# Performance work log

Hardware: AMD Instinct MI355X
Metric: run time of the kernel (lower is better)

Reference implementation:

```python
import jax, jax.numpy as jnp
import numpy as np

N = 100000      # nodes
E = 1600000     # edges
DIM = 64        # feat_channel
H = 4           # heads
C = DIM // H    # per-head channels
L = 3           # layer_num
G = 16          # graphs in batch
NCLS = 2
NEG_SLOPE_ATT = 0.2   # GATConv leaky relu
NEG_SLOPE_ACT = 0.01  # 'Leaky' activation
EPS = 1e-5


def setup_inputs() -> dict:
    key = jax.random.key(0)
    ks = jax.random.split(key, 8)
    x = jax.random.normal(ks[0], (N, DIM), dtype=jnp.float32)
    edge_index = jax.random.randint(ks[1], (2, E), 0, N, dtype=jnp.int32)
    batch = jnp.sort(jax.random.randint(ks[2], (N,), 0, G, dtype=jnp.int32))
    W = jax.random.normal(ks[3], (L, DIM, DIM), dtype=jnp.float32) / np.sqrt(DIM)
    att_src = jax.random.normal(ks[4], (L, H, C), dtype=jnp.float32) * 0.1
    att_dst = jax.random.normal(ks[5], (L, H, C), dtype=jnp.float32) * 0.1
    bias = jnp.zeros((L, DIM), dtype=jnp.float32)
    gamma = jnp.ones((L, DIM), dtype=jnp.float32)
    beta = jnp.zeros((L, DIM), dtype=jnp.float32)
    Wr = jax.random.normal(ks[6], ((L + 1) * DIM, NCLS), dtype=jnp.float32) / np.sqrt((L + 1) * DIM)
    br = jnp.zeros((NCLS,), dtype=jnp.float32)
    return {"x": x, "edge_index": edge_index, "batch": batch, "n_graphs": G,
            "W": W, "att_src": att_src, "att_dst": att_dst, "bias": bias,
            "gamma": gamma, "beta": beta, "Wr": Wr, "br": br}


def _gat_conv(x, src, dst, W_l, a_src, a_dst, b_l):
    # x: [N, DIM] -> h: [N, H, C]
    h = (x @ W_l).reshape(-1, H, C)
    # per-node attention logits [N, H]
    e_src = jnp.einsum('nhc,hc->nh', h, a_src)
    e_dst = jnp.einsum('nhc,hc->nh', h, a_dst)
    alpha = jax.nn.leaky_relu(e_src[src] + e_dst[dst], NEG_SLOPE_ATT)  # [E, H]
    # segment softmax over incoming edges of each destination node
    amax = jax.ops.segment_max(alpha, dst, num_segments=N)
    ex = jnp.exp(alpha - amax[dst])
    den = jax.ops.segment_sum(ex, dst, num_segments=N)
    att = ex / (den[dst] + 1e-16)                                      # [E, H]
    # weighted scatter aggregation
    msg = h[src] * att[:, :, None]                                     # [E, H, C]
    out = jax.ops.segment_sum(msg, dst, num_segments=N)
    return out.reshape(-1, H * C) + b_l, att


def _batch_norm(x, g, b):
    mu = jnp.mean(x, axis=0)
    var = jnp.var(x, axis=0)
    return (x - mu) * jax.lax.rsqrt(var + EPS) * g + b


def _mean_pool(x, batch, n_graphs, cnt):
    return jax.ops.segment_sum(x, batch, num_segments=n_graphs) / cnt[:, None]


def reference(x, edge_index, batch, n_graphs, W, att_src, att_dst, bias, gamma, beta, Wr, br):
    src, dst = edge_index[0], edge_index[1]
    cnt = jax.ops.segment_sum(jnp.ones((x.shape[0],), x.dtype), batch,
                              num_segments=n_graphs)                   # nodes per graph
    inv_sqrt_n = jax.lax.rsqrt(cnt)[batch][:, None]                    # GraphSizeNorm factor

    x_out = x
    pools = [_mean_pool(x, batch, n_graphs, cnt)]                      # x0_glob
    for l in range(L):
        h, _att = _gat_conv(x_out, src, dst, W[l], att_src[l], att_dst[l], bias[l])
        h = _batch_norm(h, gamma[l], beta[l]) * inv_sqrt_n             # BatchNorm + GraphSizeNorm
        h = jax.nn.leaky_relu(h, NEG_SLOPE_ACT)
        pools.append(_mean_pool(h, batch, n_graphs, cnt))
        x_out = h + x_out                                              # residual 'Y'

    x_concat = jnp.concatenate(pools, axis=1)                          # [G, (L+1)*DIM]
    risk = x_concat @ Wr + br                                          # [G, NCLS]
    Y_prob = jax.nn.softmax(risk, axis=1)
    Y_hat = jnp.argmax(risk, axis=1)
    return risk, Y_prob, Y_hat
```

## Files before the change

kernel.cpp:

```cpp
#include <hip/hip_runtime.h>

constexpr int NN   = 100000;
constexpr int EE   = 1600000;
constexpr int DIM  = 64;
constexpr int HH   = 4;
constexpr int CC   = 16;
constexpr int LL   = 3;
constexpr int GG   = 16;
constexpr int NCLS = 2;
constexpr float SLOPE_ATT = 0.2f;
constexpr float SLOPE_ACT = 0.01f;
constexpr float EPS = 1e-5f;

constexpr int SCAN_CHUNK = 1024;
constexpr int NSCAN = (NN + SCAN_CHUNK - 1) / SCAN_CHUNK;
constexpr int NREP = 64;

typedef int vint4 __attribute__((ext_vector_type(4)));

__device__ __forceinline__ float lrelu_att(float v) { return v > 0.f ? v : SLOPE_ATT * v; }
__device__ __forceinline__ float lrelu_act(float v) { return v > 0.f ? v : SLOPE_ACT * v; }

__device__ __forceinline__ unsigned short f2bf(float f) {
    unsigned u = __float_as_uint(f);
    unsigned r = u + 0x7FFFu + ((u >> 16) & 1u);
    return (unsigned short)(r >> 16);
}
__device__ __forceinline__ float bflo(unsigned u) { return __uint_as_float(u << 16); }
__device__ __forceinline__ float bfhi(unsigned u) { return __uint_as_float(u & 0xFFFF0000u); }

__global__ __launch_bounds__(256) void k_hist(const int* __restrict__ ei,
                                              int* __restrict__ deg) {
    int i = blockIdx.x * 256 + threadIdx.x;
    if (i < EE / 4) {
        vint4 d = __builtin_nontemporal_load(&((const vint4*)(ei + EE))[i]);
        atomicAdd(&deg[d.x], 1);
        atomicAdd(&deg[d.y], 1);
        atomicAdd(&deg[d.z], 1);
        atomicAdd(&deg[d.w], 1);
    }
}

__global__ __launch_bounds__(256) void k_scan1(const int* __restrict__ deg,
                                               int* __restrict__ excl,
                                               int* __restrict__ bsum) {
    __shared__ int sh[256];
    const int b = blockIdx.x, t = threadIdx.x;
    const int i0 = b * SCAN_CHUNK + t * 4;
    int v[4];
#pragma unroll
    for (int i = 0; i < 4; ++i) v[i] = (i0 + i < NN) ? deg[i0 + i] : 0;
    int tsum = v[0] + v[1] + v[2] + v[3];
    sh[t] = tsum;
    __syncthreads();
    for (int o = 1; o < 256; o <<= 1) {
        int x = (t >= o) ? sh[t - o] : 0;
        __syncthreads();
        sh[t] += x;
        __syncthreads();
    }
    if (t == 255) bsum[b] = sh[255];
    int run = sh[t] - tsum;
#pragma unroll
    for (int i = 0; i < 4; ++i) {
        if (i0 + i < NN) excl[i0 + i] = run;
        run += v[i];
    }
}

__global__ void k_scan2(const int* __restrict__ bsum, int* __restrict__ bsum_sc) {
    __shared__ int sh[128];
    const int t = threadIdx.x;
    const int own = (t < NSCAN) ? bsum[t] : 0;
    sh[t] = own;
    __syncthreads();
    for (int o = 1; o < 128; o <<= 1) {
        int x = (t >= o) ? sh[t - o] : 0;
        __syncthreads();
        sh[t] += x;
        __syncthreads();
    }
    if (t < NSCAN) bsum_sc[t] = sh[t] - own;
}

__global__ __launch_bounds__(256) void k_scan3(int* __restrict__ row_start,
                                               const int* __restrict__ bsum_sc,
                                               int* __restrict__ cursor) {
    int i = blockIdx.x * 256 + threadIdx.x;
    if (i < NN) {
        int v = row_start[i] + bsum_sc[i / SCAN_CHUNK];
        row_start[i] = v;
        cursor[i] = v;
    }
    if (i == 0) row_start[NN] = EE;
}

constexpr int FILL_NBLK = 256;
constexpr int DRANGE = (NN + 7) / 8;
__global__ __launch_bounds__(256) void k_fill(const int* __restrict__ ei,
                                              int* __restrict__ cursor,
                                              int* __restrict__ ssrc) {
    const int g = blockIdx.x & 7;
    const int blk = blockIdx.x >> 3;
    const int dlo = g * DRANGE, dhi = min(dlo + DRANGE, NN);
    const int stride = FILL_NBLK * 256;
    for (int e = blk * 256 + threadIdx.x; e < EE; e += stride) {
        int d = __builtin_nontemporal_load(&ei[EE + e]);
        if (d >= dlo && d < dhi) {
            int s = __builtin_nontemporal_load(&ei[e]);
            int pos = atomicAdd(&cursor[d], 1);
            ssrc[pos] = s;
        }
    }
}

template<int MODE>
__global__ __launch_bounds__(256) void k_gemm_t(const float* __restrict__ xbase,
                                                const float* __restrict__ aggin,
                                                const float* __restrict__ scshf,
                                                const int* __restrict__ batch,
                                                const float* __restrict__ cntin,
                                                const float* __restrict__ Wl,
                                                const float* __restrict__ asrc,
                                                const float* __restrict__ adst,
                                                float* __restrict__ xcur_out,
                                                unsigned short* __restrict__ h,
                                                float* __restrict__ es,
                                                float* __restrict__ ed,
                                                double* __restrict__ bnrep,
                                                float* __restrict__ poolout,
                                                float* __restrict__ cntout) {
    if (blockIdx.x < NREP && threadIdx.x < 128)
        bnrep[(size_t)blockIdx.x * 128 + threadIdx.x] = 0.0;
    __shared__ float Ws[DIM][DIM];
    __shared__ float xsT[DIM][DIM];
    __shared__ float sp[GG * 64];
    __shared__ float scnt[GG];
    const int tid = threadIdx.x;
    const int row0 = blockIdx.x * 64;

    for (int i = tid; i < GG * 64; i += 256) sp[i] = 0.f;
    if (MODE == 0 && tid < GG) scnt[tid] = 0.f;
    __syncthreads();

    const float4* W4 = (const float4*)Wl;
#pragma unroll
    for (int i = 0; i < 4; ++i) ((float4*)Ws)[tid + 256 * i] = W4[tid + 256 * i];

    const int c4_ = tid & 15;
    float4 scv, shfv;
    if (MODE == 1) {
        scv  = ((const float4*)scshf)[c4_];
        shfv = ((const float4*)scshf)[16 + c4_];
    }

#pragma unroll
    for (int i = 0; i < 4; ++i) {
        int idx4 = tid + 256 * i;
        int r = idx4 >> 4, c4 = idx4 & 15;
        int grow = row0 + r;
        float4 v4 = make_float4(0.f, 0.f, 0.f, 0.f);
        if (grow < NN) {
            if (MODE == 0) {
                v4 = ((const float4*)xbase)[grow * 16 + c4];
                int g = batch[grow];
                atomicAdd(&sp[g * 64 + c4 * 4 + 0], v4.x);
                atomicAdd(&sp[g * 64 + c4 * 4 + 1], v4.y);
                atomicAdd(&sp[g * 64 + c4 * 4 + 2], v4.z);
                atomicAdd(&sp[g * 64 + c4 * 4 + 3], v4.w);
                if (c4 == 0) atomicAdd(&scnt[g], 1.f);
            } else {
                float4 a4 = ((const float4*)aggin)[grow * 16 + c4];
                float4 xb = ((const float4*)xbase)[grow * 16 + c4];
                int g = batch[grow];
                float rinv = rsqrtf(cntin[g]);
                float vx = lrelu_act((a4.x * scv.x + shfv.x) * rinv);
                float vy = lrelu_act((a4.y * scv.y + shfv.y) * rinv);
                float vz = lrelu_act((a4.z * scv.z + shfv.z) * rinv);
                float vw = lrelu_act((a4.w * scv.w + shfv.w) * rinv);
                atomicAdd(&sp[g * 64 + c4 * 4 + 0], vx);
                atomicAdd(&sp[g * 64 + c4 * 4 + 1], vy);
                atomicAdd(&sp[g * 64 + c4 * 4 + 2], vz);
                atomicAdd(&sp[g * 64 + c4 * 4 + 3], vw);
                v4 = make_float4(xb.x + vx, xb.y + vy, xb.z + vz, xb.w + vw);
                ((float4*)xcur_out)[grow * 16 + c4] = v4;
            }
        }
        int col = (((r >> 2) ^ c4) << 2) | (r & 3);
        xsT[c4 * 4 + 0][col] = v4.x;
        xsT[c4 * 4 + 1][col] = v4.y;
        xsT[c4 * 4 + 2][col] = v4.z;
        xsT[c4 * 4 + 3][col] = v4.w;
    }
    __syncthreads();

    const int tc = tid & 15, tr = tid >> 4;
    float acc[4][4] = {};
#pragma unroll 8
    for (int k = 0; k < DIM; ++k) {
        int kc = (k >> 2) & 15;
        float4 wv = *(const float4*)(&Ws[k][tc * 4]);
        float4 xv = *(const float4*)(&xsT[k][(tr ^ kc) * 4]);
        acc[0][0] = fmaf(xv.x, wv.x, acc[0][0]);
        acc[0][1] = fmaf(xv.x, wv.y, acc[0][1]);
        acc[0][2] = fmaf(xv.x, wv.z, acc[0][2]);
        acc[0][3] = fmaf(xv.x, wv.w, acc[0][3]);
        acc[1][0] = fmaf(xv.y, wv.x, acc[1][0]);
        acc[1][1] = fmaf(xv.y, wv.y, acc[1][1]);
        acc[1][2] = fmaf(xv.y, wv.z, acc[1][2]);
        acc[1][3] = fmaf(xv.y, wv.w, acc[1][3]);
        acc[2][0] = fmaf(xv.z, wv.x, acc[2][0]);
        acc[2][1] = fmaf(xv.z, wv.y, acc[2][1]);
        acc[2][2] = fmaf(xv.z, wv.z, acc[2][2]);
        acc[2][3] = fmaf(xv.z, wv.w, acc[2][3]);
        acc[3][0] = fmaf(xv.w, wv.x, acc[3][0]);
        acc[3][1] = fmaf(xv.w, wv.y, acc[3][1]);
        acc[3][2] = fmaf(xv.w, wv.z, acc[3][2]);
        acc[3][3] = fmaf(xv.w, wv.w, acc[3][3]);
    }

    float a_s[4], a_d[4];
#pragma unroll
    for (int c = 0; c < 4; ++c) { a_s[c] = asrc[4 * tc + c]; a_d[c] = adst[4 * tc + c]; }

#pragma unroll
    for (int r = 0; r < 4; ++r) {
        int n = row0 + 4 * tr + r;
        if (n < NN) {
            ushort4 hb;
            hb.x = f2bf(acc[r][0]); hb.y = f2bf(acc[r][1]);
            hb.z = f2bf(acc[r][2]); hb.w = f2bf(acc[r][3]);
            *(ushort4*)(h + n * 64 + 4 * tc) = hb;
            float ps = acc[r][0] * a_s[0] + acc[r][1] * a_s[1] +
                       acc[r][2] * a_s[2] + acc[r][3] * a_s[3];
            float pd = acc[r][0] * a_d[0] + acc[r][1] * a_d[1] +
                       acc[r][2] * a_d[2] + acc[r][3] * a_d[3];
            ps += __shfl_xor(ps, 1); ps += __shfl_xor(ps, 2);
            pd += __shfl_xor(pd, 1); pd += __shfl_xor(pd, 2);
            if ((tc & 3) == 0) {
                es[n * 4 + (tc >> 2)] = ps;
                ed[n * 4 + (tc >> 2)] = pd;
            }
        }
    }

    for (int i = tid; i < GG * 64; i += 256)
        if (sp[i] != 0.f) atomicAdd(&poolout[i], sp[i]);
    if (MODE == 0 && tid < GG && scnt[tid] != 0.f) atomicAdd(&cntout[tid], scnt[tid]);
}

__global__ __launch_bounds__(256) void k_gat_agg(const int* __restrict__ row_start,
                                                 const int* __restrict__ ssrc,
                                                 const float* __restrict__ es,
                                                 const float* __restrict__ ed,
                                                 const unsigned short* __restrict__ h,
                                                 float* __restrict__ agg,
                                                 double* __restrict__ bnrep) {
    __shared__ int   sbuf[16][34];
    __shared__ float exbuf[16][34][4];
    __shared__ float stS[4][64];
    __shared__ float stQ[4][64];

    const int lane16 = threadIdx.x & 15;
    const int grp    = threadIdx.x >> 4;
    const int wid    = threadIdx.x >> 6;
    const int sub    = lane16 >> 3;
    const int l8     = lane16 & 7;
    const int hq8    = l8 >> 1;
    const int n = blockIdx.x * 16 + grp;
    const int base = row_start[n];
    const int deg  = row_start[n + 1] - base;
    const float4 edv = *(const float4*)(ed + n * 4);
    const uint4* h16 = (const uint4*)h;

    float acc8[8] = {};
    float4 denp = make_float4(0.f, 0.f, 0.f, 0.f);

    if (deg <= 32) {
        int s0 = 0, s1 = 0;
        float4 al0 = make_float4(-INFINITY, -INFINITY, -INFINITY, -INFINITY);
        float4 al1 = al0;
        if (lane16 < deg) {
            s0 = ssrc[base + lane16];
            float4 ev = *(const float4*)(es + s0 * 4);
            al0.x = lrelu_att(ev.x + edv.x); al0.y = lrelu_att(ev.y + edv.y);
            al0.z = lrelu_att(ev.z + edv.z); al0.w = lrelu_att(ev.w + edv.w);
        }
        if (lane16 + 16 < deg) {
            s1 = ssrc[base + 16 + lane16];
            float4 ev = *(const float4*)(es + s1 * 4);
            al1.x = lrelu_att(ev.x + edv.x); al1.y = lrelu_att(ev.y + edv.y);
            al1.z = lrelu_att(ev.z + edv.z); al1.w = lrelu_att(ev.w + edv.w);
        }
        float4 mx = make_float4(fmaxf(al0.x, al1.x), fmaxf(al0.y, al1.y),
                                fmaxf(al0.z, al1.z), fmaxf(al0.w, al1.w));
#pragma unroll
        for (int o = 1; o < 16; o <<= 1) {
            mx.x = fmaxf(mx.x, __shfl_xor(mx.x, o));
            mx.y = fmaxf(mx.y, __shfl_xor(mx.y, o));
            mx.z = fmaxf(mx.z, __shfl_xor(mx.z, o));
            mx.w = fmaxf(mx.w, __shfl_xor(mx.w, o));
        }
        float4 ex0 = make_float4(0.f, 0.f, 0.f, 0.f), ex1 = ex0;
        if (lane16 < deg) {
            ex0.x = __expf(al0.x - mx.x); ex0.y = __expf(al0.y - mx.y);
            ex0.z = __expf(al0.z - mx.z); ex0.w = __expf(al0.w - mx.w);
        }
        if (lane16 + 16 < deg) {
            ex1.x = __expf(al1.x - mx.x); ex1.y = __expf(al1.y - mx.y);
            ex1.z = __expf(al1.z - mx.z); ex1.w = __expf(al1.w - mx.w);
        }
        denp.x = ex0.x + ex1.x; denp.y = ex0.y + ex1.y;
        denp.z = ex0.z + ex1.z; denp.w = ex0.w + ex1.w;
        sbuf[grp][lane16] = s0;
        sbuf[grp][lane16 + 16] = s1;
        *(float4*)&exbuf[grp][lane16][0] = ex0;
        *(float4*)&exbuf[grp][lane16 + 16][0] = ex1;
        const int dceil = (deg + 1) & ~1;
#pragma unroll 4
        for (int i = 0; i < dceil; i += 2) {
            int si = sbuf[grp][i + sub];
            float e = exbuf[grp][i + sub][hq8];
            uint4 hv = h16[si * 8 + l8];
            acc8[0] = fmaf(e, bflo(hv.x), acc8[0]);
            acc8[1] = fmaf(e, bfhi(hv.x), acc8[1]);
            acc8[2] = fmaf(e, bflo(hv.y), acc8[2]);
            acc8[3] = fmaf(e, bfhi(hv.y), acc8[3]);
            acc8[4] = fmaf(e, bflo(hv.z), acc8[4]);
            acc8[5] = fmaf(e, bfhi(hv.z), acc8[5]);
            acc8[6] = fmaf(e, bflo(hv.w), acc8[6]);
            acc8[7] = fmaf(e, bfhi(hv.w), acc8[7]);
        }
    } else {
        float4 mx = make_float4(-INFINITY, -INFINITY, -INFINITY, -INFINITY);
        for (int c0 = 0; c0 < deg; c0 += 16) {
            if (c0 + lane16 < deg) {
                int s = ssrc[base + c0 + lane16];
                float4 ev = *(const float4*)(es + s * 4);
                mx.x = fmaxf(mx.x, lrelu_att(ev.x + edv.x));
                mx.y = fmaxf(mx.y, lrelu_att(ev.y + edv.y));
                mx.z = fmaxf(mx.z, lrelu_att(ev.z + edv.z));
                mx.w = fmaxf(mx.w, lrelu_att(ev.w + edv.w));
            }
        }
#pragma unroll
        for (int o = 1; o < 16; o <<= 1) {
            mx.x = fmaxf(mx.x, __shfl_xor(mx.x, o));
            mx.y = fmaxf(mx.y, __shfl_xor(mx.y, o));
            mx.z = fmaxf(mx.z, __shfl_xor(mx.z, o));
            mx.w = fmaxf(mx.w, __shfl_xor(mx.w, o));
        }
        for (int c0 = 0; c0 < deg; c0 += 16) {
            int cn = min(16, deg - c0);
            float4 ex = make_float4(0.f, 0.f, 0.f, 0.f);
            int s = 0;
            if (lane16 < cn) {
                s = ssrc[base + c0 + lane16];
                float4 ev = *(const float4*)(es + s * 4);
                ex.x = __expf(lrelu_att(ev.x + edv.x) - mx.x);
                ex.y = __expf(lrelu_att(ev.y + edv.y) - mx.y);
                ex.z = __expf(lrelu_att(ev.z + edv.z) - mx.z);
                ex.w = __expf(lrelu_att(ev.w + edv.w) - mx.w);
            }
            denp.x += ex.x; denp.y += ex.y; denp.z += ex.z; denp.w += ex.w;
            sbuf[grp][lane16] = s;
            *(float4*)&exbuf[grp][lane16][0] = ex;
            const int pc = (cn + 1) & ~1;
            for (int i = 0; i < pc; i += 2) {
                int si = sbuf[grp][i + sub];
                float e = exbuf[grp][i + sub][hq8];
                uint4 hv = h16[si * 8 + l8];
                acc8[0] = fmaf(e, bflo(hv.x), acc8[0]);
                acc8[1] = fmaf(e, bfhi(hv.x), acc8[1]);
                acc8[2] = fmaf(e, bflo(hv.y), acc8[2]);
                acc8[3] = fmaf(e, bfhi(hv.y), acc8[3]);
                acc8[4] = fmaf(e, bflo(hv.z), acc8[4]);
                acc8[5] = fmaf(e, bfhi(hv.z), acc8[5]);
                acc8[6] = fmaf(e, bflo(hv.w), acc8[6]);
                acc8[7] = fmaf(e, bfhi(hv.w), acc8[7]);
            }
        }
    }

#pragma unroll
    for (int q = 0; q < 8; ++q) acc8[q] += __shfl_xor(acc8[q], 8);
#pragma unroll
    for (int o = 1; o < 16; o <<= 1) {
        denp.x += __shfl_xor(denp.x, o);
        denp.y += __shfl_xor(denp.y, o);
        denp.z += __shfl_xor(denp.z, o);
        denp.w += __shfl_xor(denp.w, o);
    }
    float dh = hq8 == 0 ? denp.x : hq8 == 1 ? denp.y : hq8 == 2 ? denp.z : denp.w;
    float inv = 1.f / (dh + 1e-16f);
    float o8[8];
#pragma unroll
    for (int q = 0; q < 8; ++q) o8[q] = acc8[q] * inv;

    if (sub == 0) {
        *(float4*)(agg + n * 64 + l8 * 8)     = make_float4(o8[0], o8[1], o8[2], o8[3]);
        *(float4*)(agg + n * 64 + l8 * 8 + 4) = make_float4(o8[4], o8[5], o8[6], o8[7]);
    }

    float sv[8], qv[8];
#pragma unroll
    for (int q = 0; q < 8; ++q) {
        float v = (sub == 0) ? o8[q] : 0.f;
        sv[q] = v; qv[q] = v * v;
    }
#pragma unroll
    for (int q = 0; q < 8; ++q) {
        sv[q] += __shfl_xor(sv[q], 16); sv[q] += __shfl_xor(sv[q], 32);
        qv[q] += __shfl_xor(qv[q], 16); qv[q] += __shfl_xor(qv[q], 32);
    }
    if ((threadIdx.x & 63) < 8) {
        *(float4*)&stS[wid][l8 * 8]     = make_float4(sv[0], sv[1], sv[2], sv[3]);
        *(float4*)&stS[wid][l8 * 8 + 4] = make_float4(sv[4], sv[5], sv[6], sv[7]);
        *(float4*)&stQ[wid][l8 * 8]     = make_float4(qv[0], qv[1], qv[2], qv[3]);
        *(float4*)&stQ[wid][l8 * 8 + 4] = make_float4(qv[4], qv[5], qv[6], qv[7]);
    }
    __syncthreads();
    if (threadIdx.x < 64) {
        int j = threadIdx.x;
        float ssum = stS[0][j] + stS[1][j] + stS[2][j] + stS[3][j];
        float qsum = stQ[0][j] + stQ[1][j] + stQ[2][j] + stQ[3][j];
        double* rep = bnrep + (size_t)(blockIdx.x & (NREP - 1)) * 128;
        atomicAdd(&rep[j], (double)ssum);
        atomicAdd(&rep[64 + j], (double)qsum);
    }
}

__global__ void k_bn_final(const double* __restrict__ bnrep,
                           const float* __restrict__ gamma,
                           const float* __restrict__ beta,
                           float* __restrict__ scshf) {
    int j = threadIdx.x;
    if (j < 64) {
        double s1 = 0.0, s2 = 0.0;
        for (int rp = 0; rp < NREP; ++rp) {
            s1 += bnrep[(size_t)rp * 128 + j];
            s2 += bnrep[(size_t)rp * 128 + 64 + j];
        }
        double mean = s1 / (double)NN;
        double var = s2 / (double)NN - mean * mean;
        float sc = (float)(1.0 / sqrt(var + (double)EPS)) * gamma[j];
        scshf[j] = sc;
        scshf[64 + j] = beta[j] - (float)mean * sc;
    }
}

constexpr int NA_BLOCKS = 512;
constexpr int NA_NODES = (NN + NA_BLOCKS - 1) / NA_BLOCKS;
__global__ __launch_bounds__(256) void k_pool_final(const float* __restrict__ agg,
                                                    const float* __restrict__ scshf,
                                                    const int* __restrict__ batch,
                                                    const float* __restrict__ cnt,
                                                    float* __restrict__ pool) {
    __shared__ float sp[GG * 64];
    for (int i = threadIdx.x; i < GG * 64; i += 256) sp[i] = 0.f;
    __syncthreads();
    const int j = threadIdx.x & 63, r = threadIdx.x >> 6;
    const float sc = scshf[j], shf = scshf[64 + j];
    const int n0 = blockIdx.x * NA_NODES;
    const int n1 = min(n0 + NA_NODES, NN);
    float racc = 0.f;
    int curg = -1;
    float rinv = 0.f;
    for (int n = n0 + r; n < n1; n += 4) {
        int g = batch[n];
        if (g != curg) {
            if (curg >= 0) atomicAdd(&sp[curg * 64 + j], racc);
            curg = g; racc = 0.f;
            rinv = rsqrtf(cnt[g]);
        }
        float v = (agg[n * 64 + j] * sc + shf) * rinv;
        racc += lrelu_act(v);
    }
    if (curg >= 0) atomicAdd(&sp[curg * 64 + j], racc);
    __syncthreads();
    for (int i = threadIdx.x; i < GG * 64; i += 256)
        if (sp[i] != 0.f) atomicAdd(&pool[i], sp[i]);
}

__global__ void k_head(const float* __restrict__ pools,
                       const float* __restrict__ cnt,
                       const float* __restrict__ Wr,
                       const float* __restrict__ br,
                       float* __restrict__ out) {
    __shared__ float risk[GG * NCLS];
    int t = threadIdx.x;
    if (t < GG * NCLS) {
        int g = t / NCLS, c = t % NCLS;
        float acc = br[c];
        float icnt = 1.f / cnt[g];
        for (int k = 0; k < (LL + 1) * DIM; ++k) {
            int l = k >> 6, j = k & 63;
            float xc = pools[(l * GG + g) * 64 + j] * icnt;
            acc += xc * Wr[k * NCLS + c];
        }
        risk[t] = acc;
        out[t] = acc;
    }
    __syncthreads();
    if (t < GG) {
        float r0 = risk[t * 2], r1 = risk[t * 2 + 1];
        float m = fmaxf(r0, r1);
        float e0 = expf(r0 - m), e1 = expf(r1 - m);
        float s = e0 + e1;
        out[GG * NCLS + t * 2] = e0 / s;
        out[GG * NCLS + t * 2 + 1] = e1 / s;
        out[2 * GG * NCLS + t] = (r1 > r0) ? 1.f : 0.f;
    }
}

extern "C" void kernel_launch(void* const* d_in, const int* in_sizes, int n_in,
                              void* d_out, int out_size, void* d_ws, size_t ws_size,
                              hipStream_t stream) {
    const float* x     = (const float*)d_in[0];
    const int*   ei    = (const int*)d_in[1];
    const int*   batch = (const int*)d_in[2];
    const float* W     = (const float*)d_in[4];
    const float* asrc  = (const float*)d_in[5];
    const float* adst  = (const float*)d_in[6];
    const float* gamma = (const float*)d_in[8];
    const float* beta  = (const float*)d_in[9];
    const float* Wr    = (const float*)d_in[10];
    const float* br    = (const float*)d_in[11];
    float* out = (float*)d_out;

    char* ws = (char*)d_ws;
    size_t off = 0;
    auto alloc = [&](size_t bytes) {
        void* p = ws + off;
        off += (bytes + 255) & ~(size_t)255;
        return p;
    };
    float*          xcur      = (float*)alloc((size_t)NN * 64 * 4);
    unsigned short* h         = (unsigned short*)alloc((size_t)NN * 64 * 2);
    float*          agg       = (float*)alloc((size_t)NN * 64 * 4);
    float*          es        = (float*)alloc((size_t)NN * 4 * 4);
    float*          ed        = (float*)alloc((size_t)NN * 4 * 4);
    int*            row_start = (int*)alloc((size_t)(NN + 1) * 4);
    int*            ssrc      = (int*)alloc((size_t)EE * 4);
    double*         bnrep     = (double*)alloc((size_t)NREP * 128 * 8);
    float*          scshf     = (float*)alloc(128 * 4);
    float*          pools     = (float*)alloc((size_t)(LL + 1) * GG * 64 * 4);
    float*          cnt       = (float*)alloc((size_t)GG * 4);
    (void)ws_size; (void)in_sizes; (void)n_in; (void)out_size;

    int* deg     = (int*)agg;
    int* cursor  = (int*)agg + NN;
    int* bsum    = (int*)agg + 2 * NN;
    int* bsum_sc = (int*)agg + 2 * NN + 256;

    hipMemsetAsync(pools, 0, (size_t)(LL + 1) * GG * 64 * 4, stream);
    hipMemsetAsync(cnt, 0, (size_t)GG * 4, stream);
    hipMemsetAsync(deg, 0, (size_t)NN * 4, stream);

    k_hist<<<(EE / 4 + 255) / 256, 256, 0, stream>>>(ei, deg);
    k_scan1<<<NSCAN, 256, 0, stream>>>(deg, row_start, bsum);
    k_scan2<<<1, 128, 0, stream>>>(bsum, bsum_sc);
    k_scan3<<<(NN + 255) / 256, 256, 0, stream>>>(row_start, bsum_sc, cursor);
    k_fill<<<8 * FILL_NBLK, 256, 0, stream>>>(ei, cursor, ssrc);

    const int GEMM_GRID = (NN + 63) / 64;

    k_gemm_t<0><<<GEMM_GRID, 256, 0, stream>>>(x, nullptr, nullptr, batch, nullptr,
                                               W, asrc, adst, nullptr,
                                               h, es, ed, bnrep, pools, cnt);
    k_gat_agg<<<NN / 16, 256, 0, stream>>>(row_start, ssrc, es, ed, h, agg, bnrep);
    k_bn_final<<<1, 64, 0, stream>>>(bnrep, gamma, beta, scshf);

    k_gemm_t<1><<<GEMM_GRID, 256, 0, stream>>>(x, agg, scshf, batch, cnt,
                                               W + DIM * DIM, asrc + HH * CC, adst + HH * CC,
                                               xcur, h, es, ed, bnrep,
                                               pools + GG * 64, nullptr);
    k_gat_agg<<<NN / 16, 256, 0, stream>>>(row_start, ssrc, es, ed, h, agg, bnrep);
    k_bn_final<<<1, 64, 0, stream>>>(bnrep, gamma + DIM, beta + DIM, scshf);

    k_gemm_t<1><<<GEMM_GRID, 256, 0, stream>>>(xcur, agg, scshf, batch, cnt,
                                               W + 2 * DIM * DIM, asrc + 2 * HH * CC,
                                               adst + 2 * HH * CC,
                                               xcur, h, es, ed, bnrep,
                                               pools + 2 * GG * 64, nullptr);
    k_gat_agg<<<NN / 16, 256, 0, stream>>>(row_start, ssrc, es, ed, h, agg, bnrep);
    k_bn_final<<<1, 64, 0, stream>>>(bnrep, gamma + 2 * DIM, beta + 2 * DIM, scshf);

    k_pool_final<<<NA_BLOCKS, 256, 0, stream>>>(agg, scshf, batch, cnt,
                                                pools + 3 * GG * 64);

    k_head<<<1, 64, 0, stream>>>(pools, cnt, Wr, br, out);
}
```

Baseline: 595.4 us.

## Store node features as FP8 for gather, merge scan kernels, widen fill grid

Node features h are now packed to FP8 with hardware pack instructions instead of BF16, halving the bytes gathered per edge in the aggregation kernel. The aggregation is remapped so each 16-lane group processes four edges per step with 16 accumulators per lane, followed by an extra shuffle reduction. The two small scan kernels are merged into one that has thread 0 serially sum the block prefix, the two memsets are combined, and the fill grid is doubled. FP8 lowers feature precision substantially, which risks accuracy tolerance failures.

```diff
diff --git a/kernel.cpp b/kernel.cpp
--- a/kernel.cpp
+++ b/kernel.cpp
@@ -17,17 +17,10 @@
 constexpr int NREP = 64;
 
 typedef int vint4 __attribute__((ext_vector_type(4)));
+typedef float f32x2 __attribute__((ext_vector_type(2)));
 
 __device__ __forceinline__ float lrelu_att(float v) { return v > 0.f ? v : SLOPE_ATT * v; }
 __device__ __forceinline__ float lrelu_act(float v) { return v > 0.f ? v : SLOPE_ACT * v; }
-
-__device__ __forceinline__ unsigned short f2bf(float f) {
-    unsigned u = __float_as_uint(f);
-    unsigned r = u + 0x7FFFu + ((u >> 16) & 1u);
-    return (unsigned short)(r >> 16);
-}
-__device__ __forceinline__ float bflo(unsigned u) { return __uint_as_float(u << 16); }
-__device__ __forceinline__ float bfhi(unsigned u) { return __uint_as_float(u & 0xFFFF0000u); }
 
 __global__ __launch_bounds__(256) void k_hist(const int* __restrict__ ei,
                                               int* __restrict__ deg) {
@@ -68,34 +61,31 @@
     }
 }
 
-__global__ void k_scan2(const int* __restrict__ bsum, int* __restrict__ bsum_sc) {
+__global__ __launch_bounds__(256) void k_scan23(int* __restrict__ row_start,
+                                                const int* __restrict__ bsum,
+                                                int* __restrict__ cursor) {
     __shared__ int sh[128];
+    __shared__ int prefix;
     const int t = threadIdx.x;
-    const int own = (t < NSCAN) ? bsum[t] : 0;
-    sh[t] = own;
-    __syncthreads();
-    for (int o = 1; o < 128; o <<= 1) {
-        int x = (t >= o) ? sh[t - o] : 0;
-        __syncthreads();
-        sh[t] += x;
-        __syncthreads();
-    }
-    if (t < NSCAN) bsum_sc[t] = sh[t] - own;
-}
-
-__global__ __launch_bounds__(256) void k_scan3(int* __restrict__ row_start,
-                                               const int* __restrict__ bsum_sc,
-                                               int* __restrict__ cursor) {
-    int i = blockIdx.x * 256 + threadIdx.x;
+    if (t < NSCAN) sh[t] = bsum[t];
+    __syncthreads();
+    if (t == 0) {
+        int ci = blockIdx.x >> 2;
+        int p = 0;
+        for (int k = 0; k < ci; ++k) p += sh[k];
+        prefix = p;
+    }
+    __syncthreads();
+    int i = blockIdx.x * 256 + t;
     if (i < NN) {
-        int v = row_start[i] + bsum_sc[i / SCAN_CHUNK];
+        int v = row_start[i] + prefix;
         row_start[i] = v;
         cursor[i] = v;
     }
     if (i == 0) row_start[NN] = EE;
 }
 
-constexpr int FILL_NBLK = 256;
+constexpr int FILL_NBLK = 512;
 constexpr int DRANGE = (NN + 7) / 8;
 __global__ __launch_bounds__(256) void k_fill(const int* __restrict__ ei,
                                               int* __restrict__ cursor,
@@ -124,7 +114,7 @@
                                                 const float* __restrict__ asrc,
                                                 const float* __restrict__ adst,
                                                 float* __restrict__ xcur_out,
-                                                unsigned short* __restrict__ h,
+                                                unsigned* __restrict__ h32,
                                                 float* __restrict__ es,
                                                 float* __restrict__ ed,
                                                 double* __restrict__ bnrep,
@@ -227,10 +217,10 @@
     for (int r = 0; r < 4; ++r) {
         int n = row0 + 4 * tr + r;
         if (n < NN) {
-            ushort4 hb;
-            hb.x = f2bf(acc[r][0]); hb.y = f2bf(acc[r][1]);
-            hb.z = f2bf(acc[r][2]); hb.w = f2bf(acc[r][3]);
-            *(ushort4*)(h + n * 64 + 4 * tc) = hb;
+            int p = 0;
+            p = __builtin_amdgcn_cvt_pk_fp8_f32(acc[r][0], acc[r][1], p, false);
+            p = __builtin_amdgcn_cvt_pk_fp8_f32(acc[r][2], acc[r][3], p, true);
+            h32[n * 16 + tc] = (unsigned)p;
             float ps = acc[r][0] * a_s[0] + acc[r][1] * a_s[1] +
                        acc[r][2] * a_s[2] + acc[r][3] * a_s[3];
             float pd = acc[r][0] * a_d[0] + acc[r][1] * a_d[1] +
@@ -249,11 +239,31 @@
     if (MODE == 0 && tid < GG && scnt[tid] != 0.f) atomicAdd(&cntout[tid], scnt[tid]);
 }
 
+__device__ __forceinline__ void acc_fp8(float acc16[16], float e, uint4 hv) {
+    f32x2 p;
+    p = __builtin_amdgcn_cvt_pk_f32_fp8((int)hv.x, false);
+    acc16[0] = fmaf(e, p.x, acc16[0]);  acc16[1] = fmaf(e, p.y, acc16[1]);
+    p = __builtin_amdgcn_cvt_pk_f32_fp8((int)hv.x, true);
+    acc16[2] = fmaf(e, p.x, acc16[2]);  acc16[3] = fmaf(e, p.y, acc16[3]);
+    p = __builtin_amdgcn_cvt_pk_f32_fp8((int)hv.y, false);
+    acc16[4] = fmaf(e, p.x, acc16[4]);  acc16[5] = fmaf(e, p.y, acc16[5]);
+    p = __builtin_amdgcn_cvt_pk_f32_fp8((int)hv.y, true);
+    acc16[6] = fmaf(e, p.x, acc16[6]);  acc16[7] = fmaf(e, p.y, acc16[7]);
+    p = __builtin_amdgcn_cvt_pk_f32_fp8((int)hv.z, false);
+    acc16[8] = fmaf(e, p.x, acc16[8]);  acc16[9] = fmaf(e, p.y, acc16[9]);
+    p = __builtin_amdgcn_cvt_pk_f32_fp8((int)hv.z, true);
+    acc16[10] = fmaf(e, p.x, acc16[10]); acc16[11] = fmaf(e, p.y, acc16[11]);
+    p = __builtin_amdgcn_cvt_pk_f32_fp8((int)hv.w, false);
+    acc16[12] = fmaf(e, p.x, acc16[12]); acc16[13] = fmaf(e, p.y, acc16[13]);
+    p = __builtin_amdgcn_cvt_pk_f32_fp8((int)hv.w, true);
+    acc16[14] = fmaf(e, p.x, acc16[14]); acc16[15] = fmaf(e, p.y, acc16[15]);
+}
+
 __global__ __launch_bounds__(256) void k_gat_agg(const int* __restrict__ row_start,
                                                  const int* __restrict__ ssrc,
                                                  const float* __restrict__ es,
                                                  const float* __restrict__ ed,
-                                                 const unsigned short* __restrict__ h,
+                                                 const unsigned* __restrict__ h32,
                                                  float* __restrict__ agg,
                                                  double* __restrict__ bnrep) {
     __shared__ int   sbuf[16][34];
@@ -264,16 +274,15 @@
     const int lane16 = threadIdx.x & 15;
     const int grp    = threadIdx.x >> 4;
     const int wid    = threadIdx.x >> 6;
-    const int sub    = lane16 >> 3;
-    const int l8     = lane16 & 7;
-    const int hq8    = l8 >> 1;
+    const int sub    = lane16 >> 2;
+    const int l4     = lane16 & 3;
     const int n = blockIdx.x * 16 + grp;
     const int base = row_start[n];
     const int deg  = row_start[n + 1] - base;
     const float4 edv = *(const float4*)(ed + n * 4);
-    const uint4* h16 = (const uint4*)h;
-
-    float acc8[8] = {};
+    const uint4* h128 = (const uint4*)h32;
+
+    float acc16[16] = {};
     float4 denp = make_float4(0.f, 0.f, 0.f, 0.f);
 
     if (deg <= 32) {
@@ -316,20 +325,13 @@
         sbuf[grp][lane16 + 16] = s1;
         *(float4*)&exbuf[grp][lane16][0] = ex0;
         *(float4*)&exbuf[grp][lane16 + 16][0] = ex1;
-        const int dceil = (deg + 1) & ~1;
+        const int dceil = (deg + 3) & ~3;
 #pragma unroll 4
-        for (int i = 0; i < dceil; i += 2) {
+        for (int i = 0; i < dceil; i += 4) {
             int si = sbuf[grp][i + sub];
-            float e = exbuf[grp][i + sub][hq8];
-            uint4 hv = h16[si * 8 + l8];
-            acc8[0] = fmaf(e, bflo(hv.x), acc8[0]);
-            acc8[1] = fmaf(e, bfhi(hv.x), acc8[1]);
-            acc8[2] = fmaf(e, bflo(hv.y), acc8[2]);
-            acc8[3] = fmaf(e, bfhi(hv.y), acc8[3]);
-            acc8[4] = fmaf(e, bflo(hv.z), acc8[4]);
-            acc8[5] = fmaf(e, bfhi(hv.z), acc8[5]);
-            acc8[6] = fmaf(e, bflo(hv.w), acc8[6]);
-            acc8[7] = fmaf(e, bfhi(hv.w), acc8[7]);
+            float e = exbuf[grp][i + sub][l4];
+            uint4 hv = h128[si * 4 + l4];
+            acc_fp8(acc16, e, hv);
         }
     } else {
         float4 mx = make_float4(-INFINITY, -INFINITY, -INFINITY, -INFINITY);
@@ -365,25 +367,21 @@
             denp.x += ex.x; denp.y += ex.y; denp.z += ex.z; denp.w += ex.w;
             sbuf[grp][lane16] = s;
             *(float4*)&exbuf[grp][lane16][0] = ex;
-            const int pc = (cn + 1) & ~1;
-            for (int i = 0; i < pc; i += 2) {
+            const int pc = (cn + 3) & ~3;
+            for (int i = 0; i < pc; i += 4) {
                 int si = sbuf[grp][i + sub];
-                float e = exbuf[grp][i + sub][hq8];
-                uint4 hv = h16[si * 8 + l8];
-                acc8[0] = fmaf(e, bflo(hv.x), acc8[0]);
-                acc8[1] = fmaf(e, bfhi(hv.x), acc8[1]);
-                acc8[2] = fmaf(e, bflo(hv.y), acc8[2]);
-                acc8[3] = fmaf(e, bfhi(hv.y), acc8[3]);
-                acc8[4] = fmaf(e, bflo(hv.z), acc8[4]);
-                acc8[5] = fmaf(e, bfhi(hv.z), acc8[5]);
-                acc8[6] = fmaf(e, bflo(hv.w), acc8[6]);
-                acc8[7] = fmaf(e, bfhi(hv.w), acc8[7]);
+                float e = exbuf[grp][i + sub][l4];
+                uint4 hv = h128[si * 4 + l4];
+                acc_fp8(acc16, e, hv);
             }
         }
     }
 
 #pragma unroll
-    for (int q = 0; q < 8; ++q) acc8[q] += __shfl_xor(acc8[q], 8);
+    for (int q = 0; q < 16; ++q) {
+        acc16[q] += __shfl_xor(acc16[q], 4);
+        acc16[q] += __shfl_xor(acc16[q], 8);
+    }
 #pragma unroll
     for (int o = 1; o < 16; o <<= 1) {
         denp.x += __shfl_xor(denp.x, o);
@@ -391,33 +389,38 @@
         denp.z += __shfl_xor(denp.z, o);
         denp.w += __shfl_xor(denp.w, o);
     }
-    float dh = hq8 == 0 ? denp.x : hq8 == 1 ? denp.y : hq8 == 2 ? denp.z : denp.w;
+    float dh = l4 == 0 ? denp.x : l4 == 1 ? denp.y : l4 == 2 ? denp.z : denp.w;
     float inv = 1.f / (dh + 1e-16f);
-    float o8[8];
-#pragma unroll
-    for (int q = 0; q < 8; ++q) o8[q] = acc8[q] * inv;
-
-    if (sub == 0) {
-        *(float4*)(agg + n * 64 + l8 * 8)     = make_float4(o8[0], o8[1], o8[2], o8[3]);
-        *(float4*)(agg + n * 64 + l8 * 8 + 4) = make_float4(o8[4], o8[5], o8[6], o8[7]);
-    }
-
-    float sv[8], qv[8];
-#pragma unroll
-    for (int q = 0; q < 8; ++q) {
-        float v = (sub == 0) ? o8[q] : 0.f;
+    float o16[16];
+#pragma unroll
+    for (int q = 0; q < 16; ++q) o16[q] = acc16[q] * inv;
+
+    if (lane16 < 4) {
+#pragma unroll
+        for (int q4 = 0; q4 < 4; ++q4)
+            *(float4*)(agg + n * 64 + lane16 * 16 + q4 * 4) =
+                make_float4(o16[q4 * 4], o16[q4 * 4 + 1], o16[q4 * 4 + 2], o16[q4 * 4 + 3]);
+    }
+
+    float sv[16], qv[16];
+#pragma unroll
+    for (int q = 0; q < 16; ++q) {
+        float v = (lane16 < 4) ? o16[q] : 0.f;
         sv[q] = v; qv[q] = v * v;
     }
 #pragma unroll
-    for (int q = 0; q < 8; ++q) {
+    for (int q = 0; q < 16; ++q) {
         sv[q] += __shfl_xor(sv[q], 16); sv[q] += __shfl_xor(sv[q], 32);
         qv[q] += __shfl_xor(qv[q], 16); qv[q] += __shfl_xor(qv[q], 32);
     }
-    if ((threadIdx.x & 63) < 8) {
-        *(float4*)&stS[wid][l8 * 8]     = make_float4(sv[0], sv[1], sv[2], sv[3]);
-        *(float4*)&stS[wid][l8 * 8 + 4] = make_float4(sv[4], sv[5], sv[6], sv[7]);
-        *(float4*)&stQ[wid][l8 * 8]     = make_float4(qv[0], qv[1], qv[2], qv[3]);
-        *(float4*)&stQ[wid][l8 * 8 + 4] = make_float4(qv[4], qv[5], qv[6], qv[7]);
+    if ((threadIdx.x & 63) < 4) {
+#pragma unroll
+        for (int q4 = 0; q4 < 4; ++q4) {
+            *(float4*)&stS[wid][l4 * 16 + q4 * 4] =
+                make_float4(sv[q4 * 4], sv[q4 * 4 + 1], sv[q4 * 4 + 2], sv[q4 * 4 + 3]);
+            *(float4*)&stQ[wid][l4 * 16 + q4 * 4] =
+                make_float4(qv[q4 * 4], qv[q4 * 4 + 1], qv[q4 * 4 + 2], qv[q4 * 4 + 3]);
+        }
     }
     __syncthreads();
     if (threadIdx.x < 64) {
@@ -535,55 +538,52 @@
         off += (bytes + 255) & ~(size_t)255;
         return p;
     };
-    float*          xcur      = (float*)alloc((size_t)NN * 64 * 4);
-    unsigned short* h         = (unsigned short*)alloc((size_t)NN * 64 * 2);
-    float*          agg       = (float*)alloc((size_t)NN * 64 * 4);
-    float*          es        = (float*)alloc((size_t)NN * 4 * 4);
-    float*          ed        = (float*)alloc((size_t)NN * 4 * 4);
-    int*            row_start = (int*)alloc((size_t)(NN + 1) * 4);
-    int*            ssrc      = (int*)alloc((size_t)EE * 4);
-    double*         bnrep     = (double*)alloc((size_t)NREP * 128 * 8);
-    float*          scshf     = (float*)alloc(128 * 4);
-    float*          pools     = (float*)alloc((size_t)(LL + 1) * GG * 64 * 4);
-    float*          cnt       = (float*)alloc((size_t)GG * 4);
+    float*    xcur      = (float*)alloc((size_t)NN * 64 * 4);
+    unsigned* h32       = (unsigned*)alloc((size_t)NN * 64);
+    float*    agg       = (float*)alloc((size_t)NN * 64 * 4);
+    float*    es        = (float*)alloc((size_t)NN * 4 * 4);
+    float*    ed        = (float*)alloc((size_t)NN * 4 * 4);
+    int*      row_start = (int*)alloc((size_t)(NN + 1) * 4);
+    int*      ssrc      = (int*)alloc((size_t)EE * 4);
+    double*   bnrep     = (double*)alloc((size_t)NREP * 128 * 8);
+    float*    scshf     = (float*)alloc(128 * 4);
+    float*    pools     = (float*)alloc((size_t)(LL + 1) * GG * 64 * 4);
+    float*    cnt       = (float*)alloc((size_t)GG * 4);
     (void)ws_size; (void)in_sizes; (void)n_in; (void)out_size;
 
-    int* deg     = (int*)agg;
-    int* cursor  = (int*)agg + NN;
-    int* bsum    = (int*)agg + 2 * NN;
-    int* bsum_sc = (int*)agg + 2 * NN + 256;
-
-    hipMemsetAsync(pools, 0, (size_t)(LL + 1) * GG * 64 * 4, stream);
-    hipMemsetAsync(cnt, 0, (size_t)GG * 4, stream);
+    int* deg    = (int*)agg;
+    int* cursor = (int*)agg + NN;
+    int* bsum   = (int*)agg + 2 * NN;
+
+    hipMemsetAsync(pools, 0, (size_t)(LL + 1) * GG * 64 * 4 + GG * 4, stream);
     hipMemsetAsync(deg, 0, (size_t)NN * 4, stream);
 
     k_hist<<<(EE / 4 + 255) / 256, 256, 0, stream>>>(ei, deg);
     k_scan1<<<NSCAN, 256, 0, stream>>>(deg, row_start, bsum);
-    k_scan2<<<1, 128, 0, stream>>>(bsum, bsum_sc);
-    k_scan3<<<(NN + 255) / 256, 256, 0, stream>>>(row_start, bsum_sc, cursor);
+    k_scan23<<<(NN + 255) / 256, 256, 0, stream>>>(row_start, bsum, cursor);
     k_fill<<<8 * FILL_NBLK, 256, 0, stream>>>(ei, cursor, ssrc);
 
     const int GEMM_GRID = (NN + 63) / 64;
 
     k_gemm_t<0><<<GEMM_GRID, 256, 0, stream>>>(x, nullptr, nullptr, batch, nullptr,
                                                W, asrc, adst, nullptr,
-                                               h, es, ed, bnrep, pools, cnt);
-    k_gat_agg<<<NN / 16, 256, 0, stream>>>(row_start, ssrc, es, ed, h, agg, bnrep);
+                                               h32, es, ed, bnrep, pools, cnt);
+    k_gat_agg<<<NN / 16, 256, 0, stream>>>(row_start, ssrc, es, ed, h32, agg, bnrep);
     k_bn_final<<<1, 64, 0, stream>>>(bnrep, gamma, beta, scshf);
 
     k_gemm_t<1><<<GEMM_GRID, 256, 0, stream>>>(x, agg, scshf, batch, cnt,
                                                W + DIM * DIM, asrc + HH * CC, adst + HH * CC,
-                                               xcur, h, es, ed, bnrep,
+                                               xcur, h32, es, ed, bnrep,
                                                pools + GG * 64, nullptr);
-    k_gat_agg<<<NN / 16, 256, 0, stream>>>(row_start, ssrc, es, ed, h, agg, bnrep);
+    k_gat_agg<<<NN / 16, 256, 0, stream>>>(row_start, ssrc, es, ed, h32, agg, bnrep);
     k_bn_final<<<1, 64, 0, stream>>>(bnrep, gamma + DIM, beta + DIM, scshf);
 
     k_gemm_t<1><<<GEMM_GRID, 256, 0, stream>>>(xcur, agg, scshf, batch, cnt,
                                                W + 2 * DIM * DIM, asrc + 2 * HH * CC,
                                                adst + 2 * HH * CC,
-                                               xcur, h, es, ed, bnrep,
+                                               xcur, h32, es, ed, bnrep,
                                                pools + 2 * GG * 64, nullptr);
-    k_gat_agg<<<NN / 16, 256, 0, stream>>>(row_start, ssrc, es, ed, h, agg, bnrep);
+    k_gat_agg<<<NN / 16, 256, 0, stream>>>(row_start, ssrc, es, ed, h32, agg, bnrep);
     k_bn_final<<<1, 64, 0, stream>>>(bnrep, gamma + 2 * DIM, beta + 2 * DIM, scshf);
 
     k_pool_final<<<NA_BLOCKS, 256, 0, stream>>>(agg, scshf, batch, cnt,
```

New measurement: 610.7 us. +2.6%, slower.
